# Optimization experiments

Measured on AMD Instinct MI355X. Metric: run time of the kernel, lower is better.

## Reference

```python
import jax, jax.numpy as jnp
import numpy as np

EPS_LN = 1e-5
EPS_BN = 1e-5


def ln_channels(x, w, b):
    # LayerNorm2d: normalize over channel dim of NCHW
    mu = x.mean(axis=1, keepdims=True)
    var = x.var(axis=1, keepdims=True)
    return (x - mu) / jnp.sqrt(var + EPS_LN) * w[None, :, None, None] + b[None, :, None, None]


def bn_eval(x, g, b):
    # eval-mode BatchNorm2d with running_mean=0, running_var=1
    return x / jnp.sqrt(1.0 + EPS_BN) * g[None, :, None, None] + b[None, :, None, None]


def conv1x1(x, w, b):
    return jnp.einsum('bchw,oc->bohw', x, w) + b[None, :, None, None]


def q_shift(x):
    # directional shift: 4 channel quarters shifted right/left/down/up by 1 px (zero pad)
    C = x.shape[1]
    q = C // 4
    return jnp.concatenate([
        jnp.pad(x[:, 0 * q:1 * q, :, :-1], ((0, 0), (0, 0), (0, 0), (1, 0))),
        jnp.pad(x[:, 1 * q:2 * q, :, 1:], ((0, 0), (0, 0), (0, 0), (0, 1))),
        jnp.pad(x[:, 2 * q:3 * q, :-1, :], ((0, 0), (0, 0), (1, 0), (0, 0))),
        jnp.pad(x[:, 3 * q:4 * q, 1:, :], ((0, 0), (0, 0), (0, 1), (0, 0))),
    ], axis=1)


def wkv_scan(k, v, w_neg, u):
    # numerically-stable RWKV WKV recurrence. k, v: [N, T, C]; w_neg (negative decay), u: [C]
    N, T, C = k.shape

    def step(carry, kv):
        a, b, p = carry
        kt, vt = kv
        q = jnp.maximum(p, u + kt)
        e1 = jnp.exp(p - q)
        e2 = jnp.exp(u + kt - q)
        out = (e1 * a + e2 * vt) / (e1 * b + e2)
        q2 = jnp.maximum(p + w_neg, kt)
        f1 = jnp.exp(p + w_neg - q2)
        f2 = jnp.exp(kt - q2)
        return (f1 * a + f2 * vt, f1 * b + f2, q2), out

    init = (jnp.zeros((N, C), k.dtype), jnp.zeros((N, C), k.dtype), jnp.full((N, C), -1e38, k.dtype))
    _, outs = jax.lax.scan(step, init, (jnp.swapaxes(k, 0, 1), jnp.swapaxes(v, 0, 1)))
    return jnp.swapaxes(outs, 0, 1)


def shape_guided_rwkv(x, mask, mix_k, mix_v, mix_r, Wk, Wv, Wr, Wo, decay, first, kn_w, kn_b):
    B, C, H, W = x.shape
    xs = q_shift(x)
    x_sh = mask * xs + (1.0 - mask) * x  # saliency-guided shift blend
    mk = mix_k[None, :, None, None]
    mv = mix_v[None, :, None, None]
    mr = mix_r[None, :, None, None]
    xk = x * mk + x_sh * (1.0 - mk)
    xv = x * mv + x_sh * (1.0 - mv)
    xr = x * mr + x_sh * (1.0 - mr)
    k = jnp.einsum('bchw,oc->bohw', xk, Wk)
    v = jnp.einsum('bchw,oc->bohw', xv, Wv)
    sr = jax.nn.sigmoid(jnp.einsum('bchw,oc->bohw', xr, Wr))
    w_neg = -jnp.exp(decay)
    # horizontal orientation: scan each row left->right
    kh = k.transpose(0, 2, 3, 1).reshape(B * H, W, C)
    vh = v.transpose(0, 2, 3, 1).reshape(B * H, W, C)
    wkv_h = wkv_scan(kh, vh, w_neg, first).reshape(B, H, W, C).transpose(0, 3, 1, 2)
    # vertical orientation: scan each column top->bottom
    kv_ = k.transpose(0, 3, 2, 1).reshape(B * W, H, C)
    vv_ = v.transpose(0, 3, 2, 1).reshape(B * W, H, C)
    wkv_v = wkv_scan(kv_, vv_, w_neg, first).reshape(B, W, H, C).transpose(0, 3, 2, 1)
    wkv = 0.5 * (wkv_h + wkv_v)
    wkv = ln_channels(wkv, kn_w, kn_b)  # key_norm=True
    out = jnp.einsum('bchw,oc->bohw', sr * wkv, Wo)
    return x + out


def channel_fusion(x, c1_w, c1_b, bn1_g, bn1_b, c2_w, c2_b, bn2_g, bn2_b, c3_w, c3_b, bn3_g, bn3_b):
    # grouped 3x3 conv (groups=2) -> GELU -> BN -> 1x1 expand -> GELU -> BN -> 1x1 reduce -> GELU -> BN
    y = jax.lax.conv_general_dilated(x, c1_w, (1, 1), 'SAME',
                                     dimension_numbers=('NCHW', 'OIHW', 'NCHW'),
                                     feature_group_count=2) + c1_b[None, :, None, None]
    y = bn_eval(jax.nn.gelu(y, approximate=False), bn1_g, bn1_b)
    y = bn_eval(jax.nn.gelu(conv1x1(y, c2_w, c2_b), approximate=False), bn2_g, bn2_b)
    y = bn_eval(jax.nn.gelu(conv1x1(y, c3_w, c3_b), approximate=False), bn3_g, bn3_b)
    return y


def patch_expand(x, up_w, up_b, s=2):
    B, C, H, W = x.shape
    y = conv1x1(x, up_w, up_b)  # [B, Cout*s*s, H, W]
    Cout = y.shape[1] // (s * s)
    y = y.reshape(B, Cout, s, s, H, W).transpose(0, 1, 4, 2, 5, 3).reshape(B, Cout, H * s, W * s)
    return y


def setup_inputs() -> dict:
    key = jax.random.key(0)
    B, C, Cs, Cout, H, W, s = 8, 256, 512, 128, 64, 64, 2
    ks = jax.random.split(key, 32)
    sc = C ** -0.5
    inp = {
        'x': jax.random.normal(ks[0], (B, C, H, W), jnp.float32),
        'skip': jax.random.normal(ks[1], (B, Cs, H, W), jnp.float32),
        'saliency_mask': jax.random.uniform(ks[2], (B, 1, H, W), jnp.float32),
        'ln1_w': jnp.ones((C,)), 'ln1_b': jnp.zeros((C,)),
        'ln2_w': jnp.ones((C,)), 'ln2_b': jnp.zeros((C,)),
        'mix_k': jax.random.uniform(ks[3], (C,)),
        'mix_v': jax.random.uniform(ks[4], (C,)),
        'mix_r': jax.random.uniform(ks[5], (C,)),
        'Wk': jax.random.normal(ks[6], (C, C)) * sc,
        'Wv': jax.random.normal(ks[7], (C, C)) * sc,
        'Wr': jax.random.normal(ks[8], (C, C)) * sc,
        'Wo': jax.random.normal(ks[9], (C, C)) * sc,
        'decay': jax.random.normal(ks[10], (C,)) * 0.5,
        'first': jax.random.normal(ks[11], (C,)) * 0.5,
        'kn_w': jnp.ones((C,)), 'kn_b': jnp.zeros((C,)),
        'sp_w': jax.random.normal(ks[12], (C, Cs)) * (Cs ** -0.5),
        'sp_b': jnp.zeros((C,)),
        'c1_w': jax.random.normal(ks[13], (2 * C, C, 3, 3)) * ((C * 9) ** -0.5),
        'c1_b': jnp.zeros((2 * C,)),
        'bn1_g': jnp.ones((2 * C,)), 'bn1_b': jnp.zeros((2 * C,)),
        'c2_w': jax.random.normal(ks[14], (4 * C, 2 * C)) * ((2 * C) ** -0.5),
        'c2_b': jnp.zeros((4 * C,)),
        'bn2_g': jnp.ones((4 * C,)), 'bn2_b': jnp.zeros((4 * C,)),
        'c3_w': jax.random.normal(ks[15], (C, 4 * C)) * ((4 * C) ** -0.5),
        'c3_b': jnp.zeros((C,)),
        'bn3_g': jnp.ones((C,)), 'bn3_b': jnp.zeros((C,)),
        'up_w': jax.random.normal(ks[16], (Cout * s * s, C)) * sc,
        'up_b': jnp.zeros((Cout * s * s,)),
    }
    return inp


def reference(x, skip, saliency_mask, ln1_w, ln1_b, ln2_w, ln2_b, mix_k, mix_v, mix_r,
              Wk, Wv, Wr, Wo, decay, first, kn_w, kn_b, sp_w, sp_b,
              c1_w, c1_b, bn1_g, bn1_b, c2_w, c2_b, bn2_g, bn2_b, c3_w, c3_b, bn3_g, bn3_b,
              up_w, up_b):
    xn = ln_channels(x, ln1_w, ln1_b)
    x_sg = shape_guided_rwkv(xn, saliency_mask, mix_k, mix_v, mix_r, Wk, Wv, Wr, Wo,
                             decay, first, kn_w, kn_b)
    skip_feat = conv1x1(skip, sp_w, sp_b)
    x_cat = jnp.concatenate([x_sg, skip_feat], axis=1)
    x_fused = channel_fusion(x_cat, c1_w, c1_b, bn1_g, bn1_b, c2_w, c2_b, bn2_g, bn2_b,
                             c3_w, c3_b, bn3_g, bn3_b)
    x_fused = ln_channels(x_fused, ln2_w, ln2_b)
    return patch_expand(x_fused, up_w, up_b, s=2)
```

## Files before the change

### kernel.cpp

```cpp
#include <hip/hip_runtime.h>
#include <hip/hip_bf16.h>
#include <math.h>

#define B_ 8
#define C_ 256
#define P_ 4096

typedef __bf16 bf16_t;
typedef __attribute__((ext_vector_type(8))) __bf16 bf16x8;
typedef __attribute__((ext_vector_type(4))) __bf16 bf16x4;
typedef __attribute__((ext_vector_type(4))) float f32x4;

template<typename T>
__global__ __launch_bounds__(256)
void ln_stats_kernel(const T* __restrict__ in, float2* __restrict__ stats)
{
    __shared__ float sred[4][64];
    __shared__ float s2red[4][64];
    int tid = threadIdx.x;
    int wp = tid & 63, cw = tid >> 6;
    int gp = blockIdx.x * 64 + wp;
    int b  = gp >> 12, p = gp & 4095;
    size_t base = (size_t)b * 256 * 4096 + p;
    float s = 0.f, s2 = 0.f;
    #pragma unroll 8
    for (int cc = 0; cc < 64; ++cc) {
        float v = (float)in[base + (size_t)(cw * 64 + cc) * 4096];
        s += v; s2 += v * v;
    }
    sred[cw][wp] = s; s2red[cw][wp] = s2;
    __syncthreads();
    if (cw == 0) {
        s  = sred[0][wp]  + sred[1][wp]  + sred[2][wp]  + sred[3][wp];
        s2 = s2red[0][wp] + s2red[1][wp] + s2red[2][wp] + s2red[3][wp];
        float mu  = s * (1.f / 256.f);
        float var = s2 * (1.f / 256.f) - mu * mu;
        stats[gp] = make_float2(mu, 1.0f / sqrtf(var + 1e-5f));
    }
}

__global__ __launch_bounds__(256)
void qshift_mix_kernel(const float* __restrict__ x, const float2* __restrict__ st1,
                       const float* __restrict__ mask,
                       const float* __restrict__ gw, const float* __restrict__ gb,
                       const float* __restrict__ mk_, const float* __restrict__ mv_,
                       const float* __restrict__ mr_,
                       bf16_t* __restrict__ xk, bf16_t* __restrict__ xv,
                       bf16_t* __restrict__ xr)
{
    int gid = blockIdx.x * 256 + threadIdx.x;
    int g = gid << 3;
    int p = g & 4095;
    int c = (g >> 12) & 255;
    int b = g >> 20;
    int h = p >> 6, w0 = p & 63;
    float gwc = gw[c], gbc = gb[c];
    int sbase = (b << 12) + p;

    float4 x0 = *reinterpret_cast<const float4*>(&x[g]);
    float4 x1 = *reinterpret_cast<const float4*>(&x[g + 4]);
    float xv8[8] = {x0.x, x0.y, x0.z, x0.w, x1.x, x1.y, x1.z, x1.w};
    float2 s8[8];
    #pragma unroll
    for (int i = 0; i < 4; ++i) {
        float4 t = *reinterpret_cast<const float4*>(&st1[sbase + i * 2]);
        s8[2 * i]     = make_float2(t.x, t.y);
        s8[2 * i + 1] = make_float2(t.z, t.w);
    }
    float xn8[8];
    #pragma unroll
    for (int i = 0; i < 8; ++i)
        xn8[i] = (xv8[i] - s8[i].x) * s8[i].y * gwc + gbc;

    float xs8[8];
    int quad = c >> 6;
    if (quad == 0) {
        xs8[0] = 0.f;
        if (w0 > 0) {
            float xm = x[g - 1]; float2 sm = st1[sbase - 1];
            xs8[0] = (xm - sm.x) * sm.y * gwc + gbc;
        }
        #pragma unroll
        for (int i = 1; i < 8; ++i) xs8[i] = xn8[i - 1];
    } else if (quad == 1) {
        #pragma unroll
        for (int i = 0; i < 7; ++i) xs8[i] = xn8[i + 1];
        xs8[7] = 0.f;
        if (w0 + 8 < 64) {
            float xp = x[g + 8]; float2 sp = st1[sbase + 8];
            xs8[7] = (xp - sp.x) * sp.y * gwc + gbc;
        }
    } else {
        int d = (quad == 2) ? -64 : 64;
        bool ok = (quad == 2) ? (h > 0) : (h < 63);
        if (ok) {
            float4 y0 = *reinterpret_cast<const float4*>(&x[g + d]);
            float4 y1 = *reinterpret_cast<const float4*>(&x[g + d + 4]);
            float yv8[8] = {y0.x, y0.y, y0.z, y0.w, y1.x, y1.y, y1.z, y1.w};
            #pragma unroll
            for (int i = 0; i < 4; ++i) {
                float4 t = *reinterpret_cast<const float4*>(&st1[sbase + d + i * 2]);
                float2 sa = make_float2(t.x, t.y), sb = make_float2(t.z, t.w);
                xs8[2 * i]     = (yv8[2 * i]     - sa.x) * sa.y * gwc + gbc;
                xs8[2 * i + 1] = (yv8[2 * i + 1] - sb.x) * sb.y * gwc + gbc;
            }
        } else {
            #pragma unroll
            for (int i = 0; i < 8; ++i) xs8[i] = 0.f;
        }
    }

    float4 m0 = *reinterpret_cast<const float4*>(&mask[sbase]);
    float4 m1 = *reinterpret_cast<const float4*>(&mask[sbase + 4]);
    float mm[8] = {m0.x, m0.y, m0.z, m0.w, m1.x, m1.y, m1.z, m1.w};
    float xsh8[8];
    #pragma unroll
    for (int i = 0; i < 8; ++i)
        xsh8[i] = mm[i] * xs8[i] + (1.f - mm[i]) * xn8[i];

    float ak = mk_[c], av = mv_[c], ar = mr_[c];
    bf16x8 ok_, ov_, or_;
    #pragma unroll
    for (int i = 0; i < 8; ++i) {
        ok_[i] = (bf16_t)(ak * xn8[i] + (1.f - ak) * xsh8[i]);
        ov_[i] = (bf16_t)(av * xn8[i] + (1.f - av) * xsh8[i]);
        or_[i] = (bf16_t)(ar * xn8[i] + (1.f - ar) * xsh8[i]);
    }
    *reinterpret_cast<bf16x8*>(&xk[g]) = ok_;
    *reinterpret_cast<bf16x8*>(&xv[g]) = ov_;
    *reinterpret_cast<bf16x8*>(&xr[g]) = or_;
}

#define EP_NONE    0
#define EP_SIGMOID 1
#define EP_BIAS    2
#define EP_RESLN   3
#define EP_GELU_BN 4
#define EP_SHUFFLE 5
#define EP_KVR     6
#define EP_WOSKIP  7

template<int NB, int BMODE, int EPI, int OUTBF, int TILE>
__global__ __launch_bounds__(256, (TILE == 64) ? 4 : 2)
void mfma_gemm(const bf16_t* __restrict__ Wp, const void* __restrict__ Xin,
               const bf16_t* __restrict__ X2,
               const float2* __restrict__ bstats, const float* __restrict__ blnw,
               const float* __restrict__ blnb,
               const float* __restrict__ bias, const float* __restrict__ skipin,
               const float* __restrict__ bng, const float* __restrict__ bnb,
               const float* __restrict__ resx, const float2* __restrict__ estats,
               const float* __restrict__ elnw, const float* __restrict__ elnb,
               void* __restrict__ OutV,
               int O, int K, int Cstride, int obs, int ocoff)
{
    constexpr int MI = TILE / 32;
    constexpr int BROWS = (NB == 3) ? 2 * 66 : TILE;
    __shared__ bf16_t Alds[NB * TILE * 36];
    __shared__ bf16_t Blds[BROWS * 36];
    int tid = threadIdx.x;
    int bx = blockIdx.x;
    int o0 = blockIdx.y * TILE;
    int b  = blockIdx.z;
    int p0 = bx * TILE;
    int cbase = (NB == 3) ? ((o0 >> 8) << 8) : 0;

    bool wo = true;
    int bb = b;
    if (EPI == EP_WOSKIP) { wo = (b >> 3) != 0; bb = b & 7; }

    const bf16_t* Wpe = Wp;
    if (EPI == EP_KVR)    Wpe = Wp + (size_t)(b >> 3) * O * K;
    if (EPI == EP_WOSKIP) Wpe = wo ? Wp : (Wp + 65536);
    int Krun = K;
    if (EPI == EP_WOSKIP) Krun = wo ? 256 : 512;

    int lane = tid & 63, wid = tid >> 6;
    int l15 = lane & 15;
    int lk8 = (lane >> 4) << 3;
    int mbase = (wid >> 1) * (TILE / 2);
    int nbase = (wid & 1) * (TILE / 2);

    const bf16_t* Xb_bf = (const bf16_t*)Xin + (size_t)bb * Cstride * 4096;
    const float*  Xb_f  = (const float*)Xin + (size_t)bb * Cstride * 4096;
    const bf16_t* X2b   = (BMODE == 3) ? X2 + (size_t)bb * Cstride * 4096 : nullptr;
    const float*  skf   = (EPI == EP_WOSKIP)
                          ? skipin + (size_t)bb * 512 * 4096 : nullptr;

    f32x4 acc[MI][MI] = {};

    if (NB == 3 && tid < 144) {
        int r = tid / 72, rest = tid % 72;
        int col = rest / 36, cc = rest % 36;
        Blds[(r * 66 + (col ? 65 : 0)) * 36 + cc] = (bf16_t)0.f;
    }

    for (int kh = 0; kh < NB; ++kh) {
        for (int c0 = 0; c0 < Krun; c0 += 32) {
            __syncthreads();
            if (NB == 3) {
                #pragma unroll
                for (int q = 0; q < 2; ++q) {
                    int cid = tid + q * 256;
                    int r   = cid >> 8;
                    int w   = (cid >> 2) & 63;
                    int ch4 = cid & 3;
                    int hr  = (bx << 1) + kh - 1 + r;
                    bf16x8 bv;
                    #pragma unroll
                    for (int i = 0; i < 8; ++i) bv[i] = (bf16_t)0.f;
                    if (hr >= 0 && hr < 64)
                        bv = *reinterpret_cast<const bf16x8*>(
                               Xb_bf + (size_t)((hr << 6) + w) * 512
                                     + cbase + c0 + ch4 * 8);
                    *reinterpret_cast<bf16x8*>(
                        &Blds[(r * 66 + w + 1) * 36 + ch4 * 8]) = bv;
                }
            } else {
                int p_loc = tid & (TILE - 1);
                float2 st = make_float2(0.f, 1.f);
                if (BMODE >= 2 && (EPI != EP_WOSKIP || wo))
                    st = bstats[(bb << 12) + p0 + p_loc];
                #pragma unroll
                for (int rep = 0; rep < (TILE == 128 ? 2 : 1); ++rep) {
                    int cgr = (TILE == 128) ? ((tid >> 7) + rep * 2) : (tid >> 6);
                    bf16x8 bv;
                    size_t gbase = (size_t)(c0 + cgr * 8) * 4096 + p0 + p_loc;
                    #pragma unroll
                    for (int j = 0; j < 8; ++j) {
                        size_t gi = gbase + (size_t)j * 4096;
                        int cc = c0 + cgr * 8 + j;
                        if (EPI == EP_WOSKIP && !wo) {
                            bv[j] = (bf16_t)skf[gi];
                        } else if (BMODE == 0) {
                            bv[j] = Xb_bf[gi];
                        } else if (BMODE == 1) {
                            bv[j] = (bf16_t)Xb_f[gi];
                        } else {
                            float v = ((float)Xb_bf[gi] - st.x) * st.y * blnw[cc] + blnb[cc];
                            if (BMODE == 3) v *= (float)X2b[gi];
                            bv[j] = (bf16_t)v;
                        }
                    }
                    *reinterpret_cast<bf16x8*>(&Blds[p_loc * 36 + cgr * 8]) = bv;
                }
            }
            if (TILE == 128) {
                int ao = tid >> 1, aq = tid & 1;
                #pragma unroll
                for (int t = 0; t < NB; ++t) {
                    const bf16_t* wsrc = (NB == 3)
                        ? Wpe + ((size_t)(kh * 3 + t) * O + o0 + ao) * 256 + c0
                        : Wpe + (size_t)(o0 + ao) * Krun + c0;
                    bf16x8 w0 = *reinterpret_cast<const bf16x8*>(wsrc + aq * 8);
                    bf16x8 w1 = *reinterpret_cast<const bf16x8*>(wsrc + (aq + 2) * 8);
                    *reinterpret_cast<bf16x8*>(&Alds[(t * 128 + ao) * 36 + aq * 8]) = w0;
                    *reinterpret_cast<bf16x8*>(&Alds[(t * 128 + ao) * 36 + (aq + 2) * 8]) = w1;
                }
            } else {
                int ao = tid >> 2, aq = tid & 3;
                const bf16_t* wsrc = Wpe + (size_t)(o0 + ao) * Krun + c0;
                bf16x8 w0 = *reinterpret_cast<const bf16x8*>(wsrc + aq * 8);
                *reinterpret_cast<bf16x8*>(&Alds[ao * 36 + aq * 8]) = w0;
            }
            __syncthreads();
            #pragma unroll
            for (int t = 0; t < NB; ++t) {
                bf16x8 af[MI];
                #pragma unroll
                for (int i = 0; i < MI; ++i)
                    af[i] = *reinterpret_cast<const bf16x8*>(
                              &Alds[(t * TILE + mbase + i * 16 + l15) * 36 + lk8]);
                #pragma unroll
                for (int j = 0; j < MI; ++j) {
                    int pl = nbase + j * 16;
                    int baddr;
                    if (NB == 3)
                        baddr = ((pl >> 6) * 66 + (pl & 63) + l15 + t) * 36 + lk8;
                    else
                        baddr = (pl + l15) * 36 + lk8;
                    bf16x8 bfv = *reinterpret_cast<const bf16x8*>(&Blds[baddr]);
                    #pragma unroll
                    for (int i = 0; i < MI; ++i)
                        acc[i][j] = __builtin_amdgcn_mfma_f32_16x16x32_bf16(
                                        af[i], bfv, acc[i][j], 0, 0, 0);
                }
            }
        }
    }

    const float bnsc = 1.0f / sqrtf(1.f + 1e-5f);
    bool kvr_sig = (EPI == EP_KVR) && (b >= 16);

    if (EPI == EP_WOSKIP) {
        int oco = wo ? 0 : 256;
        #pragma unroll
        for (int i = 0; i < MI; ++i) {
            int ob = o0 + mbase + i * 16 + ((lane >> 4) << 2);
            float bi4[4], rw4[4], rb4[4];
            #pragma unroll
            for (int r = 0; r < 4; ++r) {
                bi4[r] = wo ? 0.f : bias[ob + r];
                rw4[r] = wo ? elnw[ob + r] : 0.f;
                rb4[r] = wo ? elnb[ob + r] : 0.f;
            }
            #pragma unroll
            for (int j = 0; j < MI; ++j) {
                int pp = p0 + nbase + j * 16 + l15;
                float2 st = make_float2(0.f, 1.f);
                if (wo) st = estats[(bb << 12) + pp];
                bf16x4 pk;
                #pragma unroll
                for (int r = 0; r < 4; ++r) {
                    float t = acc[i][j][r];
                    if (!wo) {
                        t += bi4[r];
                    } else {
                        float rv = resx[((size_t)bb * 256 + ob + r) * 4096 + pp];
                        t += (rv - st.x) * st.y * rw4[r] + rb4[r];
                    }
                    pk[r] = (bf16_t)t;
                }
                *reinterpret_cast<bf16x4*>(
                    &((bf16_t*)OutV)[((size_t)bb * 4096 + pp) * 512 + oco + ob]) = pk;
            }
        }
        return;
    }

    #pragma unroll
    for (int i = 0; i < MI; ++i) {
        #pragma unroll
        for (int r = 0; r < 4; ++r) {
            int o = o0 + mbase + i * 16 + ((lane >> 4) << 2) + r;
            float bi = 0.f;
            if (EPI == EP_BIAS || EPI == EP_GELU_BN || EPI == EP_SHUFFLE) bi = bias[o];
            float sc = 0.f, sh = 0.f;
            if (EPI == EP_GELU_BN) { sc = bng[o] * bnsc; sh = bnb[o]; }
            float rw = 0.f, rb = 0.f;
            if (EPI == EP_RESLN) { rw = elnw[o]; rb = elnb[o]; }
            #pragma unroll
            for (int j = 0; j < MI; ++j) {
                int pp = p0 + nbase + j * 16 + l15;
                float t = acc[i][j][r];
                if (EPI == EP_SIGMOID) t = 1.f / (1.f + expf(-t));
                if (EPI == EP_KVR && kvr_sig) t = 1.f / (1.f + expf(-t));
                if (EPI == EP_BIAS || EPI == EP_GELU_BN || EPI == EP_SHUFFLE) t += bi;
                if (EPI == EP_RESLN) {
                    float2 st = estats[(bb << 12) + pp];
                    float rv = resx[((size_t)bb * 256 + o) * 4096 + pp];
                    t += (rv - st.x) * st.y * rw + rb;
                }
                if (EPI == EP_GELU_BN) {
                    t = 0.5f * t * (1.f + erff(t * 0.70710678118654752f));
                    t = t * sc + sh;
                }
                if (EPI == EP_SHUFFLE) {
                    int co = o >> 2, s1 = (o >> 1) & 1, s2 = o & 1;
                    int hh = pp >> 6, ww = pp & 63;
                    ((float*)OutV)[(((size_t)bb * 128 + co) * 128 + hh * 2 + s1) * 128
                                   + ww * 2 + s2] = t;
                } else {
                    size_t oidx = ((size_t)bb * obs + ocoff + o) * 4096 + pp;
                    if (OUTBF) ((bf16_t*)OutV)[oidx] = (bf16_t)t;
                    else       ((float*)OutV)[oidx]  = t;
                }
            }
        }
    }
}

__global__ __launch_bounds__(256)
void pack_all_kernel(const float* __restrict__ wk, const float* __restrict__ wv,
                     const float* __restrict__ wr, const float* __restrict__ wo,
                     const float* __restrict__ sp, const float* __restrict__ c2,
                     const float* __restrict__ c3, const float* __restrict__ up,
                     const float* __restrict__ c1, bf16_t* __restrict__ outfl,
                     bf16_t* __restrict__ outc1)
{
    int g = blockIdx.x * 256 + threadIdx.x;
    if (g < 1310720) {
        float v;
        if      (g < 65536)   v = wk[g];
        else if (g < 131072)  v = wv[g - 65536];
        else if (g < 196608)  v = wr[g - 131072];
        else if (g < 262144)  v = wo[g - 196608];
        else if (g < 393216)  v = sp[g - 262144];
        else if (g < 917504)  v = c2[g - 393216];
        else if (g < 1179648) v = c3[g - 917504];
        else                  v = up[g - 1179648];
        outfl[g] = (bf16_t)v;
    } else {
        int g2 = g - 1310720;
        if (g2 < 1179648) {
            int c = g2 & 255;
            int o = (g2 >> 8) & 511;
            int tap = g2 >> 17;
            outc1[g2] = (bf16_t)c1[(size_t)o * 2304 + c * 9 + tap];
        }
    }
}

__global__ __launch_bounds__(64)
void wkv_h_kernel(const bf16_t* __restrict__ kin, const bf16_t* __restrict__ vin,
                  bf16_t* __restrict__ outw,
                  const float* __restrict__ decay, const float* __restrict__ first)
{
    __shared__ bf16_t ks[64 * 66];
    __shared__ bf16_t vs[64 * 66];
    int c0 = blockIdx.x * 64;
    int h  = blockIdx.y;
    int b  = blockIdx.z;
    int tid = threadIdx.x;
    size_t base = (((size_t)b * 256 + c0) * 64 + h) * 64;

    for (int f = tid; f < 64 * 64; f += 64) {
        int cc = f >> 6, w = f & 63;
        ks[cc * 66 + w] = kin[base + (size_t)cc * 4096 + w];
        vs[cc * 66 + w] = vin[base + (size_t)cc * 4096 + w];
    }
    __syncthreads();

    int c = c0 + tid;
    float u  = first[c];
    float wn = -expf(decay[c]);
    float a = 0.f, bb = 0.f, pp = -1e38f;
    for (int t = 0; t < 64; ++t) {
        float kt = (float)ks[tid * 66 + t], vt = (float)vs[tid * 66 + t];
        float q  = fmaxf(pp, u + kt);
        float e1 = expf(pp - q), e2 = expf(u + kt - q);
        float ov = (e1 * a + e2 * vt) / (e1 * bb + e2);
        ks[tid * 66 + t] = (bf16_t)ov;
        float q2 = fmaxf(pp + wn, kt);
        float f1 = expf(pp + wn - q2), f2 = expf(kt - q2);
        a = f1 * a + f2 * vt;
        bb = f1 * bb + f2;
        pp = q2;
    }
    __syncthreads();
    for (int f = tid; f < 64 * 64; f += 64) {
        int cc = f >> 6, w = f & 63;
        outw[base + (size_t)cc * 4096 + w] = ks[cc * 66 + w];
    }
}

__global__ __launch_bounds__(256)
void wkv_v_kernel(const bf16_t* __restrict__ kin, const bf16_t* __restrict__ vin,
                  bf16_t* __restrict__ outw,
                  const float* __restrict__ decay, const float* __restrict__ first)
{
    int g = blockIdx.x * 256 + threadIdx.x;
    int w = g & 63;
    int c = (g >> 6) & 255;
    int b = g >> 14;
    size_t base = (size_t)(b * 256 + c) * 4096 + w;
    float u  = first[c];
    float wn = -expf(decay[c]);
    float a = 0.f, bb = 0.f, pp = -1e38f;
    for (int h = 0; h < 64; ++h) {
        size_t idx = base + h * 64;
        float kt = (float)kin[idx], vt = (float)vin[idx];
        float q  = fmaxf(pp, u + kt);
        float e1 = expf(pp - q), e2 = expf(u + kt - q);
        float ov = (e1 * a + e2 * vt) / (e1 * bb + e2);
        outw[idx] = (bf16_t)(0.5f * ((float)outw[idx] + ov));
        float q2 = fmaxf(pp + wn, kt);
        float f1 = expf(pp + wn - q2), f2 = expf(kt - q2);
        a = f1 * a + f2 * vt;
        bb = f1 * bb + f2;
        pp = q2;
    }
}

extern "C" void kernel_launch(void* const* d_in, const int* in_sizes, int n_in,
                              void* d_out, int out_size, void* d_ws, size_t ws_size,
                              hipStream_t stream)
{
    const float* x      = (const float*)d_in[0];
    const float* skip   = (const float*)d_in[1];
    const float* mask   = (const float*)d_in[2];
    const float* ln1_w  = (const float*)d_in[3];
    const float* ln1_b  = (const float*)d_in[4];
    const float* ln2_w  = (const float*)d_in[5];
    const float* ln2_b  = (const float*)d_in[6];
    const float* mix_k  = (const float*)d_in[7];
    const float* mix_v  = (const float*)d_in[8];
    const float* mix_r  = (const float*)d_in[9];
    const float* Wk     = (const float*)d_in[10];
    const float* Wv     = (const float*)d_in[11];
    const float* Wr     = (const float*)d_in[12];
    const float* Wo     = (const float*)d_in[13];
    const float* decay  = (const float*)d_in[14];
    const float* first  = (const float*)d_in[15];
    const float* kn_w   = (const float*)d_in[16];
    const float* kn_b   = (const float*)d_in[17];
    const float* sp_w   = (const float*)d_in[18];
    const float* sp_b   = (const float*)d_in[19];
    const float* c1_w   = (const float*)d_in[20];
    const float* c1_b   = (const float*)d_in[21];
    const float* bn1_g  = (const float*)d_in[22];
    const float* bn1_b  = (const float*)d_in[23];
    const float* c2_w   = (const float*)d_in[24];
    const float* c2_b   = (const float*)d_in[25];
    const float* bn2_g  = (const float*)d_in[26];
    const float* bn2_b  = (const float*)d_in[27];
    const float* c3_w   = (const float*)d_in[28];
    const float* c3_b   = (const float*)d_in[29];
    const float* bn3_g  = (const float*)d_in[30];
    const float* bn3_b  = (const float*)d_in[31];
    const float* up_w   = (const float*)d_in[32];
    const float* up_b   = (const float*)d_in[33];
    float* out = (float*)d_out;

    float* ws = (float*)d_ws;
    const size_t S = 8388608;
    const size_t Hs = S / 2;
    bf16_t* xk   = (bf16_t*)ws;
    bf16_t* xv   = (bf16_t*)(ws + Hs);
    bf16_t* xr   = (bf16_t*)(ws + 2 * Hs);
    bf16_t* kbuf = (bf16_t*)(ws + 3 * Hs);
    bf16_t* vbuf = (bf16_t*)(ws + 4 * Hs);
    bf16_t* rbuf = (bf16_t*)(ws + 5 * Hs);
    bf16_t* wkv  = (bf16_t*)(ws + 6 * Hs);
    bf16_t* xcat = (bf16_t*)(ws + 7 * Hs);
    bf16_t* y1   = (bf16_t*)(ws + 9 * Hs);
    bf16_t* y2   = (bf16_t*)ws;
    bf16_t* y3   = (bf16_t*)(ws + 4 * Hs);
    float*  wtop = ws + 11 * Hs;
    bf16_t* w9   = (bf16_t*)wtop;
    bf16_t* wfl  = w9 + 1179648;
    float2* st1  = (float2*)(wfl + 1310720);
    float2* stk  = st1 + 32768;
    float2* st2  = stk + 32768;
    bf16_t* wkb = wfl;
    bf16_t* wob = wfl + 196608;
    bf16_t* c2b = wfl + 393216;
    bf16_t* c3b = wfl + 917504;
    bf16_t* upb = wfl + 1179648;

    dim3 blk(256);

    pack_all_kernel<<<dim3(9728), blk, 0, stream>>>(Wk, Wv, Wr, Wo, sp_w, c2_w,
                                                    c3_w, up_w, c1_w, wfl, w9);
    ln_stats_kernel<float><<<dim3(512), blk, 0, stream>>>(x, st1);

    qshift_mix_kernel<<<dim3(4096), blk, 0, stream>>>(x, st1, mask, ln1_w, ln1_b,
                                                      mix_k, mix_v, mix_r, xk, xv, xr);
    mfma_gemm<1, 0, EP_KVR, 1, 64><<<dim3(64, 4, 24), blk, 0, stream>>>(
        wkb, xk, nullptr, nullptr, nullptr, nullptr, nullptr, nullptr, nullptr,
        nullptr, nullptr, nullptr, nullptr, nullptr, kbuf, 256, 256, 256, 256, 0);
    wkv_h_kernel<<<dim3(4, 64, 8), dim3(64), 0, stream>>>(kbuf, vbuf, wkv, decay, first);
    wkv_v_kernel<<<dim3(512), blk, 0, stream>>>(kbuf, vbuf, wkv, decay, first);
    ln_stats_kernel<bf16_t><<<dim3(512), blk, 0, stream>>>(wkv, stk);
    mfma_gemm<1, 3, EP_WOSKIP, 1, 64><<<dim3(64, 4, 16), blk, 0, stream>>>(
        wob, wkv, rbuf, stk, kn_w, kn_b, sp_b, skip, nullptr, nullptr,
        x, st1, ln1_w, ln1_b, xcat, 256, 0, 256, 512, 0);
    mfma_gemm<3, 0, EP_GELU_BN, 1, 128><<<dim3(32, 4, 8), blk, 0, stream>>>(
        w9, xcat, nullptr, nullptr, nullptr, nullptr, c1_b, nullptr, bn1_g, bn1_b,
        nullptr, nullptr, nullptr, nullptr, y1, 512, 256, 512, 512, 0);
    mfma_gemm<1, 0, EP_GELU_BN, 1, 128><<<dim3(32, 8, 8), blk, 0, stream>>>(
        c2b, y1, nullptr, nullptr, nullptr, nullptr, c2_b, nullptr, bn2_g, bn2_b,
        nullptr, nullptr, nullptr, nullptr, y2, 1024, 512, 512, 1024, 0);
    mfma_gemm<1, 0, EP_GELU_BN, 1, 64><<<dim3(64, 4, 8), blk, 0, stream>>>(
        c3b, y2, nullptr, nullptr, nullptr, nullptr, c3_b, nullptr, bn3_g, bn3_b,
        nullptr, nullptr, nullptr, nullptr, y3, 256, 1024, 1024, 256, 0);
    ln_stats_kernel<bf16_t><<<dim3(512), blk, 0, stream>>>(y3, st2);
    mfma_gemm<1, 2, EP_SHUFFLE, 0, 64><<<dim3(64, 8, 8), blk, 0, stream>>>(
        upb, y3, nullptr, st2, ln2_w, ln2_b, up_b, nullptr, nullptr, nullptr,
        nullptr, nullptr, nullptr, nullptr, out, 512, 256, 256, 0, 0);
}
```

Baseline: 486.1 us.

## Store channel-fusion intermediates pixel-major for vectorized GEMM operand loads

The GELU-BN GEMM epilogues now write y1, y2 and y3 in a pixel-major [B, P, C] layout. The following GEMMs gain a new operand-load mode that reads contiguous 8-channel vectors per pixel instead of eight strided scalar loads. The LN stats pass over y3 and the final upsample GEMM (with fused LN) also switch to the transposed layout. This is meant to cut the cost of uncoalesced channel-strided gathers, in exchange for strided per-pixel bf16x4 stores in the epilogue.

```diff
diff --git a/kernel.cpp b/kernel.cpp
--- a/kernel.cpp
+++ b/kernel.cpp
@@ -11,13 +11,37 @@
 typedef __attribute__((ext_vector_type(4))) __bf16 bf16x4;
 typedef __attribute__((ext_vector_type(4))) float f32x4;
 
-template<typename T>
+template<typename T, int TRANS>
 __global__ __launch_bounds__(256)
 void ln_stats_kernel(const T* __restrict__ in, float2* __restrict__ stats)
 {
     __shared__ float sred[4][64];
     __shared__ float s2red[4][64];
     int tid = threadIdx.x;
+    if (TRANS) {
+        int wp = tid >> 2, cw = tid & 3;
+        int gp = blockIdx.x * 64 + wp;
+        const bf16_t* row = (const bf16_t*)in + (size_t)gp * 256 + cw * 64;
+        float s = 0.f, s2 = 0.f;
+        #pragma unroll
+        for (int i = 0; i < 64; i += 8) {
+            bf16x8 v = *reinterpret_cast<const bf16x8*>(&row[i]);
+            #pragma unroll
+            for (int j = 0; j < 8; ++j) {
+                float f = (float)v[j]; s += f; s2 += f * f;
+            }
+        }
+        sred[cw][wp] = s; s2red[cw][wp] = s2;
+        __syncthreads();
+        if (cw == 0) {
+            s  = sred[0][wp]  + sred[1][wp]  + sred[2][wp]  + sred[3][wp];
+            s2 = s2red[0][wp] + s2red[1][wp] + s2red[2][wp] + s2red[3][wp];
+            float mu  = s * (1.f / 256.f);
+            float var = s2 * (1.f / 256.f) - mu * mu;
+            stats[gp] = make_float2(mu, 1.0f / sqrtf(var + 1e-5f));
+        }
+        return;
+    }
     int wp = tid & 63, cw = tid >> 6;
     int gp = blockIdx.x * 64 + wp;
     int b  = gp >> 12, p = gp & 4095;
@@ -140,7 +164,7 @@
 #define EP_KVR     6
 #define EP_WOSKIP  7
 
-template<int NB, int BMODE, int EPI, int OUTBF, int TILE>
+template<int NB, int BMODE, int EPI, int OUTBF, int TILE, int OTR>
 __global__ __launch_bounds__(256, (TILE == 64) ? 4 : 2)
 void mfma_gemm(const bf16_t* __restrict__ Wp, const void* __restrict__ Xin,
                const bf16_t* __restrict__ X2,
@@ -215,10 +239,30 @@
                     *reinterpret_cast<bf16x8*>(
                         &Blds[(r * 66 + w + 1) * 36 + ch4 * 8]) = bv;
                 }
+            } else if (BMODE >= 4) {
+                constexpr int NCH = (TILE == 128) ? 2 : 1;
+                #pragma unroll
+                for (int q = 0; q < NCH; ++q) {
+                    int cid = tid + q * 256;
+                    int p   = cid >> 2;
+                    int ch4 = cid & 3;
+                    bf16x8 bv = *reinterpret_cast<const bf16x8*>(
+                        Xb_bf + (size_t)(p0 + p) * Cstride + c0 + ch4 * 8);
+                    if (BMODE == 5) {
+                        float2 st = bstats[(bb << 12) + p0 + p];
+                        #pragma unroll
+                        for (int j = 0; j < 8; ++j) {
+                            int cc = c0 + ch4 * 8 + j;
+                            bv[j] = (bf16_t)(((float)bv[j] - st.x) * st.y
+                                             * blnw[cc] + blnb[cc]);
+                        }
+                    }
+                    *reinterpret_cast<bf16x8*>(&Blds[p * 36 + ch4 * 8]) = bv;
+                }
             } else {
                 int p_loc = tid & (TILE - 1);
                 float2 st = make_float2(0.f, 1.f);
-                if (BMODE >= 2 && (EPI != EP_WOSKIP || wo))
+                if (BMODE == 3 && (EPI != EP_WOSKIP || wo))
                     st = bstats[(bb << 12) + p0 + p_loc];
                 #pragma unroll
                 for (int rep = 0; rep < (TILE == 128 ? 2 : 1); ++rep) {
@@ -233,8 +277,6 @@
                             bv[j] = (bf16_t)skf[gi];
                         } else if (BMODE == 0) {
                             bv[j] = Xb_bf[gi];
-                        } else if (BMODE == 1) {
-                            bv[j] = (bf16_t)Xb_f[gi];
                         } else {
                             float v = ((float)Xb_bf[gi] - st.x) * st.y * blnw[cc] + blnb[cc];
                             if (BMODE == 3) v *= (float)X2b[gi];
@@ -322,6 +364,34 @@
                 }
                 *reinterpret_cast<bf16x4*>(
                     &((bf16_t*)OutV)[((size_t)bb * 4096 + pp) * 512 + oco + ob]) = pk;
+            }
+        }
+        return;
+    }
+
+    if (EPI == EP_GELU_BN && OTR) {
+        #pragma unroll
+        for (int i = 0; i < MI; ++i) {
+            int ob = o0 + mbase + i * 16 + ((lane >> 4) << 2);
+            float bi4[4], sc4[4], sh4[4];
+            #pragma unroll
+            for (int r = 0; r < 4; ++r) {
+                bi4[r] = bias[ob + r];
+                sc4[r] = bng[ob + r] * bnsc;
+                sh4[r] = bnb[ob + r];
+            }
+            #pragma unroll
+            for (int j = 0; j < MI; ++j) {
+                int pp = p0 + nbase + j * 16 + l15;
+                bf16x4 pk;
+                #pragma unroll
+                for (int r = 0; r < 4; ++r) {
+                    float t = acc[i][j][r] + bi4[r];
+                    t = 0.5f * t * (1.f + erff(t * 0.70710678118654752f));
+                    pk[r] = (bf16_t)(t * sc4[r] + sh4[r]);
+                }
+                *reinterpret_cast<bf16x4*>(
+                    &((bf16_t*)OutV)[((size_t)bb * 4096 + pp) * obs + ocoff + ob]) = pk;
             }
         }
         return;
@@ -541,30 +611,30 @@
 
     pack_all_kernel<<<dim3(9728), blk, 0, stream>>>(Wk, Wv, Wr, Wo, sp_w, c2_w,
                                                     c3_w, up_w, c1_w, wfl, w9);
-    ln_stats_kernel<float><<<dim3(512), blk, 0, stream>>>(x, st1);
+    ln_stats_kernel<float, 0><<<dim3(512), blk, 0, stream>>>(x, st1);
 
     qshift_mix_kernel<<<dim3(4096), blk, 0, stream>>>(x, st1, mask, ln1_w, ln1_b,
                                                       mix_k, mix_v, mix_r, xk, xv, xr);
-    mfma_gemm<1, 0, EP_KVR, 1, 64><<<dim3(64, 4, 24), blk, 0, stream>>>(
+    mfma_gemm<1, 0, EP_KVR, 1, 64, 0><<<dim3(64, 4, 24), blk, 0, stream>>>(
         wkb, xk, nullptr, nullptr, nullptr, nullptr, nullptr, nullptr, nullptr,
         nullptr, nullptr, nullptr, nullptr, nullptr, kbuf, 256, 256, 256, 256, 0);
     wkv_h_kernel<<<dim3(4, 64, 8), dim3(64), 0, stream>>>(kbuf, vbuf, wkv, decay, first);
     wkv_v_kernel<<<dim3(512), blk, 0, stream>>>(kbuf, vbuf, wkv, decay, first);
-    ln_stats_kernel<bf16_t><<<dim3(512), blk, 0, stream>>>(wkv, stk);
-    mfma_gemm<1, 3, EP_WOSKIP, 1, 64><<<dim3(64, 4, 16), blk, 0, stream>>>(
+    ln_stats_kernel<bf16_t, 0><<<dim3(512), blk, 0, stream>>>(wkv, stk);
+    mfma_gemm<1, 3, EP_WOSKIP, 1, 64, 0><<<dim3(64, 4, 16), blk, 0, stream>>>(
         wob, wkv, rbuf, stk, kn_w, kn_b, sp_b, skip, nullptr, nullptr,
         x, st1, ln1_w, ln1_b, xcat, 256, 0, 256, 512, 0);
-    mfma_gemm<3, 0, EP_GELU_BN, 1, 128><<<dim3(32, 4, 8), blk, 0, stream>>>(
+    mfma_gemm<3, 0, EP_GELU_BN, 1, 128, 1><<<dim3(32, 4, 8), blk, 0, stream>>>(
         w9, xcat, nullptr, nullptr, nullptr, nullptr, c1_b, nullptr, bn1_g, bn1_b,
         nullptr, nullptr, nullptr, nullptr, y1, 512, 256, 512, 512, 0);
-    mfma_gemm<1, 0, EP_GELU_BN, 1, 128><<<dim3(32, 8, 8), blk, 0, stream>>>(
+    mfma_gemm<1, 4, EP_GELU_BN, 1, 128, 1><<<dim3(32, 8, 8), blk, 0, stream>>>(
         c2b, y1, nullptr, nullptr, nullptr, nullptr, c2_b, nullptr, bn2_g, bn2_b,
         nullptr, nullptr, nullptr, nullptr, y2, 1024, 512, 512, 1024, 0);
-    mfma_gemm<1, 0, EP_GELU_BN, 1, 64><<<dim3(64, 4, 8), blk, 0, stream>>>(
+    mfma_gemm<1, 4, EP_GELU_BN, 1, 64, 1><<<dim3(64, 4, 8), blk, 0, stream>>>(
         c3b, y2, nullptr, nullptr, nullptr, nullptr, c3_b, nullptr, bn3_g, bn3_b,
         nullptr, nullptr, nullptr, nullptr, y3, 256, 1024, 1024, 256, 0);
-    ln_stats_kernel<bf16_t><<<dim3(512), blk, 0, stream>>>(y3, st2);
-    mfma_gemm<1, 2, EP_SHUFFLE, 0, 64><<<dim3(64, 8, 8), blk, 0, stream>>>(
+    ln_stats_kernel<bf16_t, 1><<<dim3(512), blk, 0, stream>>>(y3, st2);
+    mfma_gemm<1, 5, EP_SHUFFLE, 0, 64, 0><<<dim3(64, 8, 8), blk, 0, stream>>>(
         upb, y3, nullptr, st2, ln2_w, ln2_b, up_b, nullptr, nullptr, nullptr,
         nullptr, nullptr, nullptr, nullptr, out, 512, 256, 256, 0, 0);
 }
```

Measured after the change: 474.7 us. 2.3% less time.
